# Performance work log

Hardware: AMD Instinct MI355X
Metric: run time of the kernel (lower is better)

The kernel has to match this reference:

```python
import jax, jax.numpy as jnp
import numpy as np

B = 524288      # pixel batch
DIN = 32        # input latent dim
H = 128         # decoder hidden dim
LD = 16         # qtz_latent_dim
NE = 512        # qtz_num_embed
BETA = 0.25     # qtz_beta


def _mlp(x, w1, b1, w2, b2):
    # BasicDecoder with 1 hidden layer: relu hidden, linear out
    h = jax.nn.relu(x @ w1 + b1)
    return h @ w2 + b2


def setup_inputs() -> dict:
    key = jax.random.key(0)
    ks = jax.random.split(key, 16)
    s = 0.05
    inp = {
        "z": jax.random.normal(ks[0], (B, 1, DIN), jnp.float32),
        # codebook init: uniform(-1/LD, 1/LD) / 10, shape [latent_dim, num_embed]
        "codebook": jax.random.uniform(ks[1], (LD, NE), jnp.float32, -1.0 / LD, 1.0 / LD) / 10.0,
        "dec_w1": jax.random.normal(ks[2], (DIN, H), jnp.float32) * s,
        "dec_b1": jax.random.normal(ks[3], (H,), jnp.float32) * s,
        "dec_w2": jax.random.normal(ks[4], (H, LD), jnp.float32) * s,
        "dec_b2": jax.random.normal(ks[5], (LD,), jnp.float32) * s,
        "sc_w1": jax.random.normal(ks[6], (DIN, H), jnp.float32) * s,
        "sc_b1": jax.random.normal(ks[7], (H,), jnp.float32) * s,
        "sc_w2": jax.random.normal(ks[8], (H, 1), jnp.float32) * s,
        "sc_b2": jax.random.normal(ks[9], (1,), jnp.float32) * s,
        "rs_w1": jax.random.normal(ks[10], (DIN, H), jnp.float32) * s,
        "rs_b1": jax.random.normal(ks[11], (H,), jnp.float32) * s,
        "rs_w2": jax.random.normal(ks[12], (H, 1), jnp.float32) * s,
        "rs_b2": jax.random.normal(ks[13], (1,), jnp.float32) * s,
    }
    return inp


def reference(z, codebook, dec_w1, dec_b1, dec_w2, dec_b2,
              sc_w1, sc_b1, sc_w2, sc_b2,
              rs_w1, rs_b1, rs_w2, rs_b2):
    z0 = z[:, 0]                                   # [B, DIN]
    scaler = _mlp(z0, sc_w1, sc_b1, sc_w2, sc_b2)[..., 0]                 # [B]
    redshift = jax.nn.relu(_mlp(z0, rs_w1, rs_b1, rs_w2, rs_b2)[..., 0])  # [B]

    zd = _mlp(z, dec_w1, dec_b1, dec_w2, dec_b2)   # [B, 1, LD]
    zf = zd.reshape(-1, LD)                        # [B, LD]

    # squared L2 distances to each codebook column: [B, NE]
    d = (jnp.sum(zf * zf, axis=1, keepdims=True)
         - 2.0 * (zf @ codebook)
         + jnp.sum(codebook * codebook, axis=0)[None, :])
    min_embed_ids = jnp.argmin(d, axis=1)          # [B]

    # one_hot @ codebook.T == gather of codebook columns
    z_q = jnp.take(codebook.T, min_embed_ids, axis=0).reshape(zd.shape)   # [B,1,LD]

    sg = jax.lax.stop_gradient
    codebook_loss = jnp.mean((sg(z_q) - zd) ** 2) + BETA * jnp.mean((z_q - sg(zd)) ** 2)

    # straight-through estimator
    z_q_st = zd + sg(z_q - zd)
    return (z_q_st, scaler, redshift, codebook_loss, min_embed_ids)
```

## Files before the change

kernel.cpp:

```cpp
#include <hip/hip_runtime.h>
#include <hip/hip_bf16.h>
#include <cstdint>

#define NB    524288
#define NDIN  32
#define NH    128
#define NLD   16
#define NNE   512

#define OFF_ZQ   0
#define OFF_SC   8388608
#define OFF_RS   8912896
#define OFF_LOSS 9437184
#define OFF_IDS  9437185

#define WS_LOSS 0
#define WS_W1D  64
#define WS_W1S  (64 + 4096)
#define WS_W1R  (64 + 8192)
#define WS_CBT  (64 + 12288)
#define WS_C2   (64 + 12288 + 8192)

typedef float v2f __attribute__((ext_vector_type(2)));

static __device__ __forceinline__ v2f mk2(float a, float b) { v2f r; r[0] = a; r[1] = b; return r; }
static __device__ __forceinline__ v2f bc2(float s) { return mk2(s, s); }
static __device__ __forceinline__ v2f vfma2(v2f a, v2f b, v2f c) { return __builtin_elementwise_fma(a, b, c); }
static __device__ __forceinline__ v2f vmax0(v2f a) { return __builtin_elementwise_max(a, mk2(0.0f, 0.0f)); }

__global__ __launch_bounds__(256) void prep_kernel(
    const float* __restrict__ cb,
    const float* __restrict__ w1d, const float* __restrict__ w1s,
    const float* __restrict__ w1r, float* __restrict__ ws)
{
    int gid = blockIdx.x * 256 + threadIdx.x;
    if (gid == 0) ws[WS_LOSS] = 0.0f;
    if (gid < 4096) {
        int j = gid >> 5, k = gid & 31;
        ws[WS_W1D + gid] = w1d[k * NH + j];
        ws[WS_W1S + gid] = w1s[k * NH + j];
        ws[WS_W1R + gid] = w1r[k * NH + j];
    } else if (gid < 4096 + 8192) {
        int idx = gid - 4096;
        int j = idx >> 4, k = idx & 15;
        ws[WS_CBT + idx] = cb[k * NNE + j];
    } else if (gid < 4096 + 8192 + 512) {
        int j = gid - (4096 + 8192);
        float t[16];
#pragma unroll
        for (int k = 0; k < 16; ++k) {
            float c = cb[k * NNE + j];
            t[k] = __fmul_rn(c, c);
        }
        float r8[8];
#pragma unroll
        for (int m = 0; m < 8; ++m) r8[m] = __fadd_rn(t[m], t[m + 8]);
        float acc = __fadd_rn(
            __fadd_rn(__fadd_rn(r8[0], r8[1]), __fadd_rn(r8[2], r8[3])),
            __fadd_rn(__fadd_rn(r8[4], r8[5]), __fadd_rn(r8[6], r8[7])));
        ws[WS_C2 + j] = acc;
    }
}

__global__ __launch_bounds__(256, 4) void main_kernel(
    const float* __restrict__ z,
    const float* __restrict__ b1d, const float* __restrict__ w2d, const float* __restrict__ b2d,
    const float* __restrict__ b1s, const float* __restrict__ w2s, const float* __restrict__ b2s,
    const float* __restrict__ b1r, const float* __restrict__ w2r, const float* __restrict__ b2r,
    const float* __restrict__ ws,
    float* __restrict__ loss_acc,
    float* __restrict__ out)
{
#pragma clang fp contract(off)
    const int i  = blockIdx.x * 256 + threadIdx.x;
    const int r0 = 2 * i;

    const float* __restrict__ w1dT = ws + WS_W1D;
    const float* __restrict__ w1sT = ws + WS_W1S;
    const float* __restrict__ w1rT = ws + WS_W1R;
    const float* __restrict__ cbT  = ws + WS_CBT;
    const float* __restrict__ c2   = ws + WS_C2;

    v2f x2[32];
    {
        const float4* zv = reinterpret_cast<const float4*>(z) + (size_t)r0 * 8;
#pragma unroll
        for (int m = 0; m < 8; ++m) {
            float4 a = zv[m];
            float4 b = zv[m + 8];
            x2[4*m+0] = mk2(a.x, b.x);
            x2[4*m+1] = mk2(a.y, b.y);
            x2[4*m+2] = mk2(a.z, b.z);
            x2[4*m+3] = mk2(a.w, b.w);
        }
    }

    v2f zd2[16];
#pragma unroll
    for (int l = 0; l < 16; ++l) zd2[l] = mk2(0.0f, 0.0f);
    v2f sacc2 = mk2(0.0f, 0.0f), racc2 = mk2(0.0f, 0.0f);

    for (int j = 0; j < NH; ++j) {
        v2f hd2 = mk2(0.0f, 0.0f), hs2 = mk2(0.0f, 0.0f), hr2 = mk2(0.0f, 0.0f);
        const float* wd  = w1dT + j * 32;
        const float* wsr = w1sT + j * 32;
        const float* wr  = w1rT + j * 32;
#pragma unroll
        for (int k = 0; k < 32; ++k) {
            hd2 = vfma2(x2[k], bc2(wd[k]),  hd2);
            hs2 = vfma2(x2[k], bc2(wsr[k]), hs2);
            hr2 = vfma2(x2[k], bc2(wr[k]),  hr2);
        }
        hd2 = vmax0(hd2 + bc2(b1d[j]));
        hs2 = vmax0(hs2 + bc2(b1s[j]));
        hr2 = vmax0(hr2 + bc2(b1r[j]));
        const float* w2row = w2d + j * 16;
#pragma unroll
        for (int l = 0; l < 16; ++l) zd2[l] = vfma2(hd2, bc2(w2row[l]), zd2[l]);
        sacc2 = vfma2(hs2, bc2(w2s[j]), sacc2);
        racc2 = vfma2(hr2, bc2(w2r[j]), racc2);
    }
#pragma unroll
    for (int l = 0; l < 16; ++l) zd2[l] = zd2[l] + bc2(b2d[l]);

    v2f scaler2   = sacc2 + bc2(b2s[0]);
    v2f redshift2 = vmax0(racc2 + bc2(b2r[0]));

    v2f s2;
    {
        v2f q0 = zd2[0]  * zd2[0],  q8  = zd2[8]  * zd2[8];
        v2f q1 = zd2[1]  * zd2[1],  q9  = zd2[9]  * zd2[9];
        v2f q2 = zd2[2]  * zd2[2],  q10 = zd2[10] * zd2[10];
        v2f q3 = zd2[3]  * zd2[3],  q11 = zd2[11] * zd2[11];
        v2f q4 = zd2[4]  * zd2[4],  q12 = zd2[12] * zd2[12];
        v2f q5 = zd2[5]  * zd2[5],  q13 = zd2[13] * zd2[13];
        v2f q6 = zd2[6]  * zd2[6],  q14 = zd2[14] * zd2[14];
        v2f q7 = zd2[7]  * zd2[7],  q15 = zd2[15] * zd2[15];
        v2f r0v = q0 + q8,  r1v = q1 + q9,  r2v = q2 + q10, r3v = q3 + q11;
        v2f r4v = q4 + q12, r5v = q5 + q13, r6v = q6 + q14, r7v = q7 + q15;
        s2 = ((r0v + r1v) + (r2v + r3v)) + ((r4v + r5v) + (r6v + r7v));
    }

    float best0 = 3.4028235e38f, best1 = 3.4028235e38f;
    int bid0 = 0, bid1 = 0;
#pragma unroll 2
    for (int j = 0; j < NNE; ++j) {
        const float* cj = cbT + j * 16;
        v2f b2 = zd2[0] * bc2(cj[0]);
#pragma unroll
        for (int k = 1; k < 16; ++k) b2 = vfma2(zd2[k], bc2(cj[k]), b2);
        v2f dj2 = (s2 - bc2(2.0f) * b2) + bc2(c2[j]);
        float d0 = dj2[0], d1 = dj2[1];
        bool t0 = d0 < best0; best0 = t0 ? d0 : best0; bid0 = t0 ? j : bid0;
        bool t1 = d1 < best1; best1 = t1 ? d1 : best1; bid1 = t1 ? j : bid1;
    }

    float lsum = 0.0f;
    float4* ozq = reinterpret_cast<float4*>(out) + (size_t)r0 * 4;
    {
        const float4* cq = reinterpret_cast<const float4*>(cbT + bid0 * 16);
#pragma unroll
        for (int m = 0; m < 4; ++m) {
            float4 q = cq[m];
            float z0v = zd2[4*m+0][0], z1v = zd2[4*m+1][0], z2v = zd2[4*m+2][0], z3v = zd2[4*m+3][0];
            float e0 = __fsub_rn(q.x, z0v), e1 = __fsub_rn(q.y, z1v);
            float e2 = __fsub_rn(q.z, z2v), e3 = __fsub_rn(q.w, z3v);
            lsum = __fmaf_rn(e0, e0, lsum); lsum = __fmaf_rn(e1, e1, lsum);
            lsum = __fmaf_rn(e2, e2, lsum); lsum = __fmaf_rn(e3, e3, lsum);
            ozq[m] = make_float4(__fadd_rn(z0v, e0), __fadd_rn(z1v, e1),
                                 __fadd_rn(z2v, e2), __fadd_rn(z3v, e3));
        }
    }
    {
        const float4* cq = reinterpret_cast<const float4*>(cbT + bid1 * 16);
#pragma unroll
        for (int m = 0; m < 4; ++m) {
            float4 q = cq[m];
            float z0v = zd2[4*m+0][1], z1v = zd2[4*m+1][1], z2v = zd2[4*m+2][1], z3v = zd2[4*m+3][1];
            float e0 = __fsub_rn(q.x, z0v), e1 = __fsub_rn(q.y, z1v);
            float e2 = __fsub_rn(q.z, z2v), e3 = __fsub_rn(q.w, z3v);
            lsum = __fmaf_rn(e0, e0, lsum); lsum = __fmaf_rn(e1, e1, lsum);
            lsum = __fmaf_rn(e2, e2, lsum); lsum = __fmaf_rn(e3, e3, lsum);
            ozq[4 + m] = make_float4(__fadd_rn(z0v, e0), __fadd_rn(z1v, e1),
                                     __fadd_rn(z2v, e2), __fadd_rn(z3v, e3));
        }
    }

    *reinterpret_cast<float2*>(out + OFF_SC  + r0) = make_float2(scaler2[0],   scaler2[1]);
    *reinterpret_cast<float2*>(out + OFF_RS  + r0) = make_float2(redshift2[0], redshift2[1]);
    *reinterpret_cast<float2*>(out + OFF_IDS + r0) = make_float2((float)bid0,  (float)bid1);

#pragma unroll
    for (int off = 32; off > 0; off >>= 1) lsum += __shfl_down(lsum, off);
    __shared__ float red[4];
    if ((threadIdx.x & 63) == 0) red[threadIdx.x >> 6] = lsum;
    __syncthreads();
    if (threadIdx.x == 0)
        atomicAdd(loss_acc, red[0] + red[1] + red[2] + red[3]);
}

__global__ void fin_kernel(const float* __restrict__ ws, float* __restrict__ out) {
    float m = ws[WS_LOSS] / 8388608.0f;
    out[OFF_LOSS] = m + 0.25f * m;
}

extern "C" void kernel_launch(void* const* d_in, const int* in_sizes, int n_in,
                              void* d_out, int out_size, void* d_ws, size_t ws_size,
                              hipStream_t stream)
{
    const float* z      = (const float*)d_in[0];
    const float* cb     = (const float*)d_in[1];
    const float* dec_w1 = (const float*)d_in[2];
    const float* dec_b1 = (const float*)d_in[3];
    const float* dec_w2 = (const float*)d_in[4];
    const float* dec_b2 = (const float*)d_in[5];
    const float* sc_w1  = (const float*)d_in[6];
    const float* sc_b1  = (const float*)d_in[7];
    const float* sc_w2  = (const float*)d_in[8];
    const float* sc_b2  = (const float*)d_in[9];
    const float* rs_w1  = (const float*)d_in[10];
    const float* rs_b1  = (const float*)d_in[11];
    const float* rs_w2  = (const float*)d_in[12];
    const float* rs_b2  = (const float*)d_in[13];

    float* ws = (float*)d_ws;
    float* out = (float*)d_out;

    prep_kernel<<<50, 256, 0, stream>>>(cb, dec_w1, sc_w1, rs_w1, ws);
    main_kernel<<<NB / 2 / 256, 256, 0, stream>>>(
        z,
        dec_b1, dec_w2, dec_b2,
        sc_b1,  sc_w2,  sc_b2,
        rs_b1,  rs_w2,  rs_b2,
        ws, ws + WS_LOSS, out);
    fin_kernel<<<1, 1, 0, stream>>>(ws, out);
}
```

Measured before the change: 401.4 us.

## Split MLP and VQ search into separate kernels, stage codebook in LDS

The fused kernel becomes two. An MLP kernel writes the decoded latents into the z_q output slot. A VQ kernel with 512-thread blocks first copies the transposed codebook and its squared norms into shared memory, then reloads the latents and runs the argmin search and loss. The aim is to serve the 512-entry codebook scan from LDS instead of global/scalar loads and to lower register pressure in each kernel. In exchange the latents make an extra round trip through global memory and there is one more kernel launch.

```diff
diff --git a/kernel.cpp b/kernel.cpp
--- a/kernel.cpp
+++ b/kernel.cpp
@@ -62,13 +62,12 @@
     }
 }
 
-__global__ __launch_bounds__(256, 4) void main_kernel(
+__global__ __launch_bounds__(256, 4) void mlp_kernel(
     const float* __restrict__ z,
     const float* __restrict__ b1d, const float* __restrict__ w2d, const float* __restrict__ b2d,
     const float* __restrict__ b1s, const float* __restrict__ w2s, const float* __restrict__ b2s,
     const float* __restrict__ b1r, const float* __restrict__ w2r, const float* __restrict__ b2r,
     const float* __restrict__ ws,
-    float* __restrict__ loss_acc,
     float* __restrict__ out)
 {
 #pragma clang fp contract(off)
@@ -78,8 +77,6 @@
     const float* __restrict__ w1dT = ws + WS_W1D;
     const float* __restrict__ w1sT = ws + WS_W1S;
     const float* __restrict__ w1rT = ws + WS_W1R;
-    const float* __restrict__ cbT  = ws + WS_CBT;
-    const float* __restrict__ c2   = ws + WS_C2;
 
     v2f x2[32];
     {
@@ -126,18 +123,62 @@
     v2f scaler2   = sacc2 + bc2(b2s[0]);
     v2f redshift2 = vmax0(racc2 + bc2(b2r[0]));
 
+    float4* ozq = reinterpret_cast<float4*>(out) + (size_t)r0 * 4;
+#pragma unroll
+    for (int m = 0; m < 4; ++m) {
+        ozq[m]     = make_float4(zd2[4*m+0][0], zd2[4*m+1][0], zd2[4*m+2][0], zd2[4*m+3][0]);
+        ozq[4 + m] = make_float4(zd2[4*m+0][1], zd2[4*m+1][1], zd2[4*m+2][1], zd2[4*m+3][1]);
+    }
+
+    *reinterpret_cast<float2*>(out + OFF_SC + r0) = make_float2(scaler2[0],   scaler2[1]);
+    *reinterpret_cast<float2*>(out + OFF_RS + r0) = make_float2(redshift2[0], redshift2[1]);
+}
+
+__global__ __launch_bounds__(512, 4) void vq_kernel(
+    const float* __restrict__ ws,
+    float* __restrict__ loss_acc,
+    float* __restrict__ out)
+{
+#pragma clang fp contract(off)
+    __shared__ float lcb[NNE * 16];
+    __shared__ float lc2[NNE];
+    __shared__ float red[8];
+
+    const int t = threadIdx.x;
+    {
+        const float* __restrict__ cbT = ws + WS_CBT;
+        const float* __restrict__ c2  = ws + WS_C2;
+#pragma unroll
+        for (int m = 0; m < 16; ++m) lcb[t + m * 512] = cbT[t + m * 512];
+        lc2[t & 511] = c2[t & 511];
+    }
+    __syncthreads();
+
+    const int i  = blockIdx.x * 512 + t;
+    const int r0 = 2 * i;
+
+    v2f zd2[16];
+    float4* ozq = reinterpret_cast<float4*>(out) + (size_t)r0 * 4;
+#pragma unroll
+    for (int m = 0; m < 4; ++m) {
+        float4 a = ozq[m];
+        float4 b = ozq[4 + m];
+        zd2[4*m+0] = mk2(a.x, b.x);
+        zd2[4*m+1] = mk2(a.y, b.y);
+        zd2[4*m+2] = mk2(a.z, b.z);
+        zd2[4*m+3] = mk2(a.w, b.w);
+    }
+
     v2f s2;
     {
-        v2f q0 = zd2[0]  * zd2[0],  q8  = zd2[8]  * zd2[8];
-        v2f q1 = zd2[1]  * zd2[1],  q9  = zd2[9]  * zd2[9];
-        v2f q2 = zd2[2]  * zd2[2],  q10 = zd2[10] * zd2[10];
-        v2f q3 = zd2[3]  * zd2[3],  q11 = zd2[11] * zd2[11];
-        v2f q4 = zd2[4]  * zd2[4],  q12 = zd2[12] * zd2[12];
-        v2f q5 = zd2[5]  * zd2[5],  q13 = zd2[13] * zd2[13];
-        v2f q6 = zd2[6]  * zd2[6],  q14 = zd2[14] * zd2[14];
-        v2f q7 = zd2[7]  * zd2[7],  q15 = zd2[15] * zd2[15];
-        v2f r0v = q0 + q8,  r1v = q1 + q9,  r2v = q2 + q10, r3v = q3 + q11;
-        v2f r4v = q4 + q12, r5v = q5 + q13, r6v = q6 + q14, r7v = q7 + q15;
+        v2f r0v = (zd2[0]*zd2[0]) + (zd2[8]*zd2[8]);
+        v2f r1v = (zd2[1]*zd2[1]) + (zd2[9]*zd2[9]);
+        v2f r2v = (zd2[2]*zd2[2]) + (zd2[10]*zd2[10]);
+        v2f r3v = (zd2[3]*zd2[3]) + (zd2[11]*zd2[11]);
+        v2f r4v = (zd2[4]*zd2[4]) + (zd2[12]*zd2[12]);
+        v2f r5v = (zd2[5]*zd2[5]) + (zd2[13]*zd2[13]);
+        v2f r6v = (zd2[6]*zd2[6]) + (zd2[14]*zd2[14]);
+        v2f r7v = (zd2[7]*zd2[7]) + (zd2[15]*zd2[15]);
         s2 = ((r0v + r1v) + (r2v + r3v)) + ((r4v + r5v) + (r6v + r7v));
     }
 
@@ -145,26 +186,25 @@
     int bid0 = 0, bid1 = 0;
 #pragma unroll 2
     for (int j = 0; j < NNE; ++j) {
-        const float* cj = cbT + j * 16;
+        const float* cj = lcb + j * 16;
         v2f b2 = zd2[0] * bc2(cj[0]);
 #pragma unroll
         for (int k = 1; k < 16; ++k) b2 = vfma2(zd2[k], bc2(cj[k]), b2);
-        v2f dj2 = (s2 - bc2(2.0f) * b2) + bc2(c2[j]);
+        v2f dj2 = (s2 - (b2 + b2)) + bc2(lc2[j]);
         float d0 = dj2[0], d1 = dj2[1];
         bool t0 = d0 < best0; best0 = t0 ? d0 : best0; bid0 = t0 ? j : bid0;
         bool t1 = d1 < best1; best1 = t1 ? d1 : best1; bid1 = t1 ? j : bid1;
     }
 
     float lsum = 0.0f;
-    float4* ozq = reinterpret_cast<float4*>(out) + (size_t)r0 * 4;
-    {
-        const float4* cq = reinterpret_cast<const float4*>(cbT + bid0 * 16);
+    {
+        const float* cq = lcb + bid0 * 16;
 #pragma unroll
         for (int m = 0; m < 4; ++m) {
-            float4 q = cq[m];
+            float q0 = cq[4*m+0], q1 = cq[4*m+1], q2 = cq[4*m+2], q3 = cq[4*m+3];
             float z0v = zd2[4*m+0][0], z1v = zd2[4*m+1][0], z2v = zd2[4*m+2][0], z3v = zd2[4*m+3][0];
-            float e0 = __fsub_rn(q.x, z0v), e1 = __fsub_rn(q.y, z1v);
-            float e2 = __fsub_rn(q.z, z2v), e3 = __fsub_rn(q.w, z3v);
+            float e0 = __fsub_rn(q0, z0v), e1 = __fsub_rn(q1, z1v);
+            float e2 = __fsub_rn(q2, z2v), e3 = __fsub_rn(q3, z3v);
             lsum = __fmaf_rn(e0, e0, lsum); lsum = __fmaf_rn(e1, e1, lsum);
             lsum = __fmaf_rn(e2, e2, lsum); lsum = __fmaf_rn(e3, e3, lsum);
             ozq[m] = make_float4(__fadd_rn(z0v, e0), __fadd_rn(z1v, e1),
@@ -172,13 +212,13 @@
         }
     }
     {
-        const float4* cq = reinterpret_cast<const float4*>(cbT + bid1 * 16);
+        const float* cq = lcb + bid1 * 16;
 #pragma unroll
         for (int m = 0; m < 4; ++m) {
-            float4 q = cq[m];
+            float q0 = cq[4*m+0], q1 = cq[4*m+1], q2 = cq[4*m+2], q3 = cq[4*m+3];
             float z0v = zd2[4*m+0][1], z1v = zd2[4*m+1][1], z2v = zd2[4*m+2][1], z3v = zd2[4*m+3][1];
-            float e0 = __fsub_rn(q.x, z0v), e1 = __fsub_rn(q.y, z1v);
-            float e2 = __fsub_rn(q.z, z2v), e3 = __fsub_rn(q.w, z3v);
+            float e0 = __fsub_rn(q0, z0v), e1 = __fsub_rn(q1, z1v);
+            float e2 = __fsub_rn(q2, z2v), e3 = __fsub_rn(q3, z3v);
             lsum = __fmaf_rn(e0, e0, lsum); lsum = __fmaf_rn(e1, e1, lsum);
             lsum = __fmaf_rn(e2, e2, lsum); lsum = __fmaf_rn(e3, e3, lsum);
             ozq[4 + m] = make_float4(__fadd_rn(z0v, e0), __fadd_rn(z1v, e1),
@@ -186,17 +226,18 @@
         }
     }
 
-    *reinterpret_cast<float2*>(out + OFF_SC  + r0) = make_float2(scaler2[0],   scaler2[1]);
-    *reinterpret_cast<float2*>(out + OFF_RS  + r0) = make_float2(redshift2[0], redshift2[1]);
-    *reinterpret_cast<float2*>(out + OFF_IDS + r0) = make_float2((float)bid0,  (float)bid1);
+    *reinterpret_cast<float2*>(out + OFF_IDS + r0) = make_float2((float)bid0, (float)bid1);
 
 #pragma unroll
     for (int off = 32; off > 0; off >>= 1) lsum += __shfl_down(lsum, off);
-    __shared__ float red[4];
-    if ((threadIdx.x & 63) == 0) red[threadIdx.x >> 6] = lsum;
+    if ((t & 63) == 0) red[t >> 6] = lsum;
     __syncthreads();
-    if (threadIdx.x == 0)
-        atomicAdd(loss_acc, red[0] + red[1] + red[2] + red[3]);
+    if (t == 0) {
+        float acc = 0.0f;
+#pragma unroll
+        for (int m = 0; m < 8; ++m) acc += red[m];
+        atomicAdd(loss_acc, acc);
+    }
 }
 
 __global__ void fin_kernel(const float* __restrict__ ws, float* __restrict__ out) {
@@ -227,11 +268,12 @@
     float* out = (float*)d_out;
 
     prep_kernel<<<50, 256, 0, stream>>>(cb, dec_w1, sc_w1, rs_w1, ws);
-    main_kernel<<<NB / 2 / 256, 256, 0, stream>>>(
+    mlp_kernel<<<NB / 2 / 256, 256, 0, stream>>>(
         z,
         dec_b1, dec_w2, dec_b2,
         sc_b1,  sc_w2,  sc_b2,
         rs_b1,  rs_w2,  rs_b2,
-        ws, ws + WS_LOSS, out);
+        ws, out);
+    vq_kernel<<<NB / 2 / 512, 512, 0, stream>>>(ws, ws + WS_LOSS, out);
     fin_kernel<<<1, 1, 0, stream>>>(ws, out);
 }
```

Result: slower. 417.0 us (+3.9%).
